# Kernel optimization log

Hardware: AMD Instinct MI355X
Metric: run time of the kernel (lower is better)

Reference implementation:

```python
import jax, jax.numpy as jnp
import numpy as np

N = 2_000_000
IN_CH = 10
UNITS = 32  # out_channels // 2 since last_vfe=False
KMAX = 64   # voxel coordinate range per axis


def setup_inputs() -> dict:
    key = jax.random.key(0)
    k1, k2, k3, k4, k5, k6, k7 = jax.random.split(key, 7)
    return {
        "inputs": jax.random.normal(k1, (N, IN_CH), dtype=jnp.float32),
        "mean": jax.random.normal(k2, (N, 6), dtype=jnp.float32),
        "linear_w": jax.random.normal(k3, (IN_CH, UNITS), dtype=jnp.float32) * 0.1,
        "linear_b": jax.random.normal(k4, (UNITS,), dtype=jnp.float32) * 0.1,
        "weight_w": jax.random.normal(k5, (6, UNITS), dtype=jnp.float32) * 0.1,
        "weight_b": jax.random.normal(k6, (UNITS,), dtype=jnp.float32) * 0.1,
        "bxyz_indx": jax.random.randint(k7, (N, 4), 0, KMAX, dtype=jnp.int32),
    }


def _encode_rows(bxyz_indx):
    # unique-by-row is equivalent to unique on a collision-free scalar key;
    # scatter_max-then-gather is invariant to how unique ids are labeled.
    b = bxyz_indx.astype(jnp.int64)
    return ((b[:, 0] * KMAX + b[:, 1]) * KMAX + b[:, 2]) * KMAX + b[:, 3]


def reference(inputs, mean, linear_w, linear_b, weight_w, weight_b, bxyz_indx):
    # x = relu(Linear(inputs)); gating by relu(Linear(mean))  (activate=True, gs=None)
    x = jax.nn.relu(inputs @ linear_w + linear_b)          # [N, UNITS]
    x_weight = jax.nn.relu(mean @ weight_w + weight_b)     # [N, UNITS]
    x = x * x_weight
    # unique voxel id per point -> inverse indices (jit-safe fixed size)
    keys = _encode_rows(bxyz_indx)
    _, inv = jnp.unique(keys, return_inverse=True, size=keys.shape[0], fill_value=-1)
    inv = inv.reshape(-1)
    # scatter_max over voxels, then gather back per point
    max_feature = jax.ops.segment_max(x, inv, num_segments=keys.shape[0])
    gather_max = max_feature[inv, :]                       # [N, UNITS]
    return jnp.concatenate([x, gather_max], axis=1)        # [N, 2*UNITS]
```

## Files before the change

### kernel.cpp

```cpp
#include <hip/hip_runtime.h>
#include <stdint.h>

#define IN_CH   10
#define MEAN_CH 6
#define UNITS   32
#define KEYSPACE (1 << 24)

typedef float f32x4 __attribute__((ext_vector_type(4)));

__device__ __forceinline__ unsigned key_hash(int key, int cshift, unsigned cmask) {
    return (((unsigned)key * 2654435761u) >> cshift) & cmask;
}

__global__ __launch_bounds__(256) void vfe_count(
    const int* __restrict__ bxyz, unsigned* __restrict__ seen,
    unsigned* __restrict__ multi, int* __restrict__ keys, int nrows)
{
    int row = blockIdx.x * blockDim.x + threadIdx.x;
    if (row >= nrows) return;
    const int4 b = *(const int4*)(bxyz + (size_t)row * 4);
    int key = ((b.x * 64 + b.y) * 64 + b.z) * 64 + b.w;
    keys[row] = key;
    unsigned w = (unsigned)key >> 5, bit = 1u << (key & 31);
    unsigned old = atomicOr(&seen[w], bit);
    if (old & bit) atomicOr(&multi[w], bit);
}

__global__ __launch_bounds__(256) void vfe_compute(
    const float* __restrict__ inputs, const float* __restrict__ mean,
    const float* __restrict__ W1, const float* __restrict__ b1,
    const float* __restrict__ W2, const float* __restrict__ b2,
    const int* __restrict__ keys, const unsigned* __restrict__ multi,
    int* __restrict__ ktab, float* __restrict__ out, int* __restrict__ maxtab,
    unsigned cmask, int cshift, int nrows)
{
    __shared__ float smem[576];
    for (int i = threadIdx.x; i < 576; i += 256) {
        float v;
        if      (i < 320) v = W1[i];
        else if (i < 352) v = b1[i - 320];
        else if (i < 544) v = W2[i - 352];
        else              v = b2[i - 544];
        smem[i] = v;
    }
    __syncthreads();
    const float* sW1 = smem;
    const float* sb1 = smem + 320;
    const float* sW2 = smem + 352;
    const float* sb2 = smem + 544;

    int tid   = blockIdx.x * blockDim.x + threadIdx.x;
    int row   = tid >> 3;
    int lane8 = tid & 7;
    int c4    = lane8 * 4;
    if (row >= nrows) return;

    int key = keys[row];
    bool is_multi = (multi[(unsigned)key >> 5] >> (key & 31)) & 1;

    const float2* __restrict__ ip = (const float2*)(inputs + (size_t)row * IN_CH);
    const float2* __restrict__ mp = (const float2*)(mean   + (size_t)row * MEAN_CH);

    float4 bb1 = *(const float4*)(sb1 + c4);
    float a0 = bb1.x, a1 = bb1.y, a2 = bb1.z, a3 = bb1.w;
#pragma unroll
    for (int k2 = 0; k2 < IN_CH / 2; ++k2) {
        float2 v  = ip[k2];
        float4 wA = *(const float4*)(sW1 + (2 * k2)     * UNITS + c4);
        float4 wB = *(const float4*)(sW1 + (2 * k2 + 1) * UNITS + c4);
        a0 = fmaf(v.x, wA.x, a0); a1 = fmaf(v.x, wA.y, a1);
        a2 = fmaf(v.x, wA.z, a2); a3 = fmaf(v.x, wA.w, a3);
        a0 = fmaf(v.y, wB.x, a0); a1 = fmaf(v.y, wB.y, a1);
        a2 = fmaf(v.y, wB.z, a2); a3 = fmaf(v.y, wB.w, a3);
    }
    a0 = fmaxf(a0, 0.0f); a1 = fmaxf(a1, 0.0f);
    a2 = fmaxf(a2, 0.0f); a3 = fmaxf(a3, 0.0f);

    float4 bb2 = *(const float4*)(sb2 + c4);
    float g0 = bb2.x, g1 = bb2.y, g2 = bb2.z, g3 = bb2.w;
#pragma unroll
    for (int k2 = 0; k2 < MEAN_CH / 2; ++k2) {
        float2 v  = mp[k2];
        float4 wA = *(const float4*)(sW2 + (2 * k2)     * UNITS + c4);
        float4 wB = *(const float4*)(sW2 + (2 * k2 + 1) * UNITS + c4);
        g0 = fmaf(v.x, wA.x, g0); g1 = fmaf(v.x, wA.y, g1);
        g2 = fmaf(v.x, wA.z, g2); g3 = fmaf(v.x, wA.w, g3);
        g0 = fmaf(v.y, wB.x, g0); g1 = fmaf(v.y, wB.y, g1);
        g2 = fmaf(v.y, wB.z, g2); g3 = fmaf(v.y, wB.w, g3);
    }
    g0 = fmaxf(g0, 0.0f); g1 = fmaxf(g1, 0.0f);
    g2 = fmaxf(g2, 0.0f); g3 = fmaxf(g3, 0.0f);

    f32x4 x;
    x.x = a0 * g0; x.y = a1 * g1; x.z = a2 * g2; x.w = a3 * g3;

    *(f32x4*)(out + (size_t)row * 64 + c4) = x;
    if (!is_multi) {
        *(f32x4*)(out + (size_t)row * 64 + 32 + c4) = x;
    } else {
        int slot;
        if (lane8 == 0) {
            unsigned h = key_hash(key, cshift, cmask);
            int tag = key + 1;
            while (true) {
                int old = atomicCAS(&ktab[h], 0, tag);
                if (old == 0 || old == tag) break;
                h = (h + 1) & cmask;
            }
            slot = (int)h;
        }
        slot = __shfl(slot, 0, 8);
        int* __restrict__ mt = maxtab + (size_t)slot * UNITS + c4;
        atomicMax(mt + 0, (int)__float_as_uint(x.x));
        atomicMax(mt + 1, (int)__float_as_uint(x.y));
        atomicMax(mt + 2, (int)__float_as_uint(x.z));
        atomicMax(mt + 3, (int)__float_as_uint(x.w));
    }
}

__global__ __launch_bounds__(256) void vfe_fixup(
    const int* __restrict__ keys, const unsigned* __restrict__ multi,
    const int* __restrict__ ktab, const int* __restrict__ maxtab,
    float* __restrict__ out, unsigned cmask, int cshift, int nrows)
{
    int row = blockIdx.x * blockDim.x + threadIdx.x;
    if (row >= nrows) return;
    int key = keys[row];
    if (!((multi[(unsigned)key >> 5] >> (key & 31)) & 1)) return;
    unsigned h = key_hash(key, cshift, cmask);
    int tag = key + 1;
    while (ktab[h] != tag) h = (h + 1) & cmask;
    const f32x4* src = (const f32x4*)(maxtab + (size_t)h * UNITS);
    f32x4* dst = (f32x4*)(out + (size_t)row * 64 + 32);
#pragma unroll
    for (int i = 0; i < 8; ++i) dst[i] = src[i];
}

extern "C" void kernel_launch(void* const* d_in, const int* in_sizes, int n_in,
                              void* d_out, int out_size, void* d_ws, size_t ws_size,
                              hipStream_t stream)
{
    const float* inputs = (const float*)d_in[0];
    const float* mean   = (const float*)d_in[1];
    const float* W1     = (const float*)d_in[2];
    const float* b1     = (const float*)d_in[3];
    const float* W2     = (const float*)d_in[4];
    const float* b2     = (const float*)d_in[5];
    const int*   bxyz   = (const int*)d_in[6];
    float* out = (float*)d_out;

    const int nrows = in_sizes[0] / IN_CH;

    const size_t BMWORDS = KEYSPACE / 32;
    unsigned cbits = 20;
    size_t need = BMWORDS * 8
                + ((size_t)1 << cbits) * 4
                + (size_t)nrows * 4
                + ((size_t)1 << cbits) * UNITS * 4;
    if (need > ws_size) cbits = 19;
    const size_t CSIZE = (size_t)1 << cbits;
    const unsigned cmask = (unsigned)(CSIZE - 1);
    const int cshift = 32 - (int)cbits;

    char* p = (char*)d_ws;
    unsigned* seen  = (unsigned*)p;  p += BMWORDS * 4;
    unsigned* multi = (unsigned*)p;  p += BMWORDS * 4;
    int* ktab       = (int*)p;       p += CSIZE * 4;
    int* keys       = (int*)p;       p += (size_t)nrows * 4;
    int* maxtab     = (int*)p;

    (void)hipMemsetAsync(seen, 0, BMWORDS * 8 + CSIZE * 4, stream);

    const int blk = 256;
    vfe_count<<<(nrows + blk - 1) / blk, blk, 0, stream>>>(
        bxyz, seen, multi, keys, nrows);

    const int total = nrows * 8;
    vfe_compute<<<(total + blk - 1) / blk, blk, 0, stream>>>(
        inputs, mean, W1, b1, W2, b2, keys, multi,
        ktab, out, maxtab, cmask, cshift, nrows);

    vfe_fixup<<<(nrows + blk - 1) / blk, blk, 0, stream>>>(
        keys, multi, ktab, maxtab, out, cmask, cshift, nrows);
}
```

Before: 840.0 us.

## Replace seen/multi bitmaps with byte counters and widen fixup to 8 lanes

```diff
diff --git a/kernel.cpp b/kernel.cpp
--- a/kernel.cpp
+++ b/kernel.cpp
@@ -13,17 +13,34 @@
 }
 
 __global__ __launch_bounds__(256) void vfe_count(
-    const int* __restrict__ bxyz, unsigned* __restrict__ seen,
-    unsigned* __restrict__ multi, int* __restrict__ keys, int nrows)
+    const int* __restrict__ bxyz, unsigned* __restrict__ cnt_words,
+    int* __restrict__ keys, int nrows)
 {
     int row = blockIdx.x * blockDim.x + threadIdx.x;
     if (row >= nrows) return;
     const int4 b = *(const int4*)(bxyz + (size_t)row * 4);
     int key = ((b.x * 64 + b.y) * 64 + b.z) * 64 + b.w;
     keys[row] = key;
-    unsigned w = (unsigned)key >> 5, bit = 1u << (key & 31);
-    unsigned old = atomicOr(&seen[w], bit);
-    if (old & bit) atomicOr(&multi[w], bit);
+    atomicAdd(&cnt_words[key >> 2], 1u << ((key & 3) * 8));
+}
+
+__global__ __launch_bounds__(256) void vfe_multiscan(
+    const unsigned* __restrict__ cnt_words, unsigned* __restrict__ multi,
+    int nwords)
+{
+    int i = blockIdx.x * blockDim.x + threadIdx.x;
+    if (i >= nwords) return;
+    const int4* cw = (const int4*)cnt_words + (size_t)i * 2;
+    int4 w0 = cw[0], w1 = cw[1];
+    unsigned w[8] = {(unsigned)w0.x, (unsigned)w0.y, (unsigned)w0.z, (unsigned)w0.w,
+                     (unsigned)w1.x, (unsigned)w1.y, (unsigned)w1.z, (unsigned)w1.w};
+    unsigned bits = 0;
+#pragma unroll
+    for (int j = 0; j < 8; ++j)
+#pragma unroll
+        for (int bb = 0; bb < 4; ++bb)
+            if (((w[j] >> (8 * bb)) & 0xFFu) > 1u) bits |= 1u << (j * 4 + bb);
+    multi[i] = bits;
 }
 
 __global__ __launch_bounds__(256) void vfe_compute(
@@ -123,17 +140,22 @@
     const int* __restrict__ ktab, const int* __restrict__ maxtab,
     float* __restrict__ out, unsigned cmask, int cshift, int nrows)
 {
-    int row = blockIdx.x * blockDim.x + threadIdx.x;
+    int tid   = blockIdx.x * blockDim.x + threadIdx.x;
+    int row   = tid >> 3;
+    int lane8 = tid & 7;
     if (row >= nrows) return;
     int key = keys[row];
     if (!((multi[(unsigned)key >> 5] >> (key & 31)) & 1)) return;
-    unsigned h = key_hash(key, cshift, cmask);
-    int tag = key + 1;
-    while (ktab[h] != tag) h = (h + 1) & cmask;
-    const f32x4* src = (const f32x4*)(maxtab + (size_t)h * UNITS);
-    f32x4* dst = (f32x4*)(out + (size_t)row * 64 + 32);
-#pragma unroll
-    for (int i = 0; i < 8; ++i) dst[i] = src[i];
+    int slot;
+    if (lane8 == 0) {
+        unsigned h = key_hash(key, cshift, cmask);
+        int tag = key + 1;
+        while (ktab[h] != tag) h = (h + 1) & cmask;
+        slot = (int)h;
+    }
+    slot = __shfl(slot, 0, 8);
+    f32x4 v = *(const f32x4*)(maxtab + (size_t)slot * UNITS + lane8 * 4);
+    *(f32x4*)(out + (size_t)row * 64 + 32 + lane8 * 4) = v;
 }
 
 extern "C" void kernel_launch(void* const* d_in, const int* in_sizes, int n_in,
@@ -151,10 +173,11 @@
 
     const int nrows = in_sizes[0] / IN_CH;
 
-    const size_t BMWORDS = KEYSPACE / 32;
+    const int BMW = KEYSPACE / 32;
     unsigned cbits = 20;
-    size_t need = BMWORDS * 8
+    size_t need = (size_t)KEYSPACE
                 + ((size_t)1 << cbits) * 4
+                + (size_t)BMW * 4
                 + (size_t)nrows * 4
                 + ((size_t)1 << cbits) * UNITS * 4;
     if (need > ws_size) cbits = 19;
@@ -163,23 +186,26 @@
     const int cshift = 32 - (int)cbits;
 
     char* p = (char*)d_ws;
-    unsigned* seen  = (unsigned*)p;  p += BMWORDS * 4;
-    unsigned* multi = (unsigned*)p;  p += BMWORDS * 4;
-    int* ktab       = (int*)p;       p += CSIZE * 4;
-    int* keys       = (int*)p;       p += (size_t)nrows * 4;
-    int* maxtab     = (int*)p;
-
-    (void)hipMemsetAsync(seen, 0, BMWORDS * 8 + CSIZE * 4, stream);
+    unsigned* cnt_words = (unsigned*)p;  p += KEYSPACE;
+    int* ktab           = (int*)p;       p += CSIZE * 4;
+    unsigned* multi     = (unsigned*)p;  p += (size_t)BMW * 4;
+    int* keys           = (int*)p;       p += (size_t)nrows * 4;
+    int* maxtab         = (int*)p;
+
+    (void)hipMemsetAsync(cnt_words, 0, (size_t)KEYSPACE + CSIZE * 4, stream);
 
     const int blk = 256;
     vfe_count<<<(nrows + blk - 1) / blk, blk, 0, stream>>>(
-        bxyz, seen, multi, keys, nrows);
+        bxyz, cnt_words, keys, nrows);
+
+    vfe_multiscan<<<(BMW + blk - 1) / blk, blk, 0, stream>>>(
+        cnt_words, multi, BMW);
 
     const int total = nrows * 8;
     vfe_compute<<<(total + blk - 1) / blk, blk, 0, stream>>>(
         inputs, mean, W1, b1, W2, b2, keys, multi,
         ktab, out, maxtab, cmask, cshift, nrows);
 
-    vfe_fixup<<<(nrows + blk - 1) / blk, blk, 0, stream>>>(
+    vfe_fixup<<<(total + blk - 1) / blk, blk, 0, stream>>>(
         keys, multi, ktab, maxtab, out, cmask, cshift, nrows);
 }
```

Result: no change. 853.7 us (+1.6%).
